# Performance work log

Hardware: AMD Instinct MI355X
Metric: run time of the kernel (lower is better)

## Reference

```python
import jax, jax.numpy as jnp
import numpy as np

CUBE_SIZE = 24
N_NEURONS = CUBE_SIZE ** 3  # 13824
INPUT_DIM = 512
OUTPUT_DIM = 1000
MAX_STEPS = 30
BATCH = 256


def _build_neighbor_indices(size: int) -> np.ndarray:
    """[N, 27] int32; invalid (out-of-cube) neighbors map to pad slot N."""
    n = size ** 3
    c = np.arange(size)
    z, y, x = np.meshgrid(c, c, c, indexing='ij')  # each [size,size,size]
    cols = []
    for dz in (-1, 0, 1):
        for dy in (-1, 0, 1):
            for dx in (-1, 0, 1):
                nz, ny, nx = z + dz, y + dy, x + dx
                valid = ((nz >= 0) & (nz < size) & (ny >= 0) & (ny < size)
                         & (nx >= 0) & (nx < size))
                idx = nz * size * size + ny * size + nx
                cols.append(np.where(valid, idx, n))
    return np.stack(cols, axis=-1).reshape(n, 27).astype(np.int32)


def setup_inputs() -> dict:
    key = jax.random.key(0)
    ks = jax.random.split(key, 4)
    # xavier-ish small init scales (gain 0.5 style)
    w_in = jax.random.normal(ks[0], (N_NEURONS, INPUT_DIM), jnp.float32) * 0.01
    w_local = jax.random.normal(ks[1], (N_NEURONS, 27), jnp.float32) * 0.1
    w_out = jax.random.normal(ks[2], (OUTPUT_DIM, N_NEURONS), jnp.float32) * 0.01
    x = jax.random.normal(ks[3], (BATCH, INPUT_DIM), jnp.float32)
    return {
        'x': x,
        'W_in_w': w_in,
        'W_in_b': jnp.zeros((N_NEURONS,), jnp.float32),
        'W_local': w_local,
        'W_out_w': w_out,
        'W_out_b': jnp.zeros((OUTPUT_DIM,), jnp.float32),
        'neighbor_indices': jnp.asarray(_build_neighbor_indices(CUBE_SIZE)),
    }


def reference(x, W_in_w, W_in_b, W_local, W_out_w, W_out_b, neighbor_indices):
    batch = x.shape[0]
    x_proj = x @ W_in_w.T + W_in_b  # [B, N]
    h0 = jnp.zeros((batch, N_NEURONS), x.dtype)
    pad = jnp.zeros((batch, 1), x.dtype)

    def step(h, _):
        h_padded = jnp.concatenate([h, pad], axis=1)        # [B, N+1]
        nbr = h_padded[:, neighbor_indices]                  # [B, N, 27]
        weighted = jnp.einsum('bnk,nk->bn', nbr, W_local)    # [B, N]
        return jnp.tanh(x_proj + weighted), None

    h, _ = jax.lax.scan(step, h0, None, length=MAX_STEPS)
    return h @ W_out_w.T + W_out_b  # [B, output_dim]
```

## Files before the change

### kernel.cpp

```cpp
#include <hip/hip_runtime.h>

#define NN   13824
#define BB   256
#define KDIM 512
#define ODIM 1000
#define CUBE 24
#define KS   16

typedef short bf8 __attribute__((ext_vector_type(8)));
typedef float f32x4 __attribute__((ext_vector_type(4)));

__device__ __forceinline__ float fast_tanh(float a) {
    float e = __expf(2.0f * a);
    return 1.0f - 2.0f / (e + 1.0f);
}
__device__ __forceinline__ float bf_lo(unsigned u) { return __uint_as_float(u << 16); }
__device__ __forceinline__ float bf_hi(unsigned u) { return __uint_as_float(u & 0xffff0000u); }
__device__ __forceinline__ unsigned short bf_rne(float f) {
    unsigned u = __float_as_uint(f);
    u += 0x7fffu + ((u >> 16) & 1u);
    return (unsigned short)(u >> 16);
}
__device__ __forceinline__ unsigned bf_pack(float lo, float hi) {
    return (unsigned)bf_rne(lo) | ((unsigned)bf_rne(hi) << 16);
}
__device__ __forceinline__ bf8 cvt8(float4 a, float4 b) {
    bf8 r;
    r[0] = (short)bf_rne(a.x); r[1] = (short)bf_rne(a.y);
    r[2] = (short)bf_rne(a.z); r[3] = (short)bf_rne(a.w);
    r[4] = (short)bf_rne(b.x); r[5] = (short)bf_rne(b.y);
    r[6] = (short)bf_rne(b.z); r[7] = (short)bf_rne(b.w);
    return r;
}

__global__ __launch_bounds__(256) void xbf_kernel(
    const float* __restrict__ x, unsigned* __restrict__ xb)
{
    int i = blockIdx.x * 256 + threadIdx.x;
    float2 v = *(const float2*)&x[(size_t)i * 2];
    xb[i] = bf_pack(v.x, v.y);
}

__global__ __launch_bounds__(256) void xproj_mfma(
    const float* __restrict__ w_in, const float* __restrict__ bias,
    const short* __restrict__ xbf, unsigned short* __restrict__ xp)
{
    const int tid = threadIdx.x, w = tid >> 6, lane = tid & 63;
    const int quad = lane >> 4, l16 = lane & 15;
    const int n0 = blockIdx.x * 16;
    const float* __restrict__ arow = &w_in[(size_t)(n0 + l16) * KDIM];

    f32x4 acc[4] = {};
    for (int k0 = 0; k0 < KDIM; k0 += 32) {
        const int ka = k0 + quad * 8;
        float4 a0 = *(const float4*)&arow[ka];
        float4 a1 = *(const float4*)&arow[ka + 4];
        bf8 af = cvt8(a0, a1);
#pragma unroll
        for (int j = 0; j < 4; ++j) {
            const int b = w * 64 + j * 16 + l16;
            bf8 bfr = *(const bf8*)&xbf[(size_t)b * KDIM + ka];
            acc[j] = __builtin_amdgcn_mfma_f32_16x16x32_bf16(af, bfr, acc[j], 0, 0, 0);
        }
    }
#pragma unroll
    for (int j = 0; j < 4; ++j) {
        const int b = w * 64 + j * 16 + l16;
#pragma unroll
        for (int r = 0; r < 4; ++r) {
            const int n = n0 + quad * 4 + r;
            xp[(size_t)n * BB + b] = bf_rne(acc[j][r] + bias[n]);
        }
    }
}

__global__ __launch_bounds__(256) void init_kernel(
    const unsigned* __restrict__ xp, unsigned* __restrict__ h)
{
    int i = (blockIdx.x * 256 + threadIdx.x) * 4;
    uint4 v = *(const uint4*)&xp[i];
    uint4 o;
    o.x = bf_pack(fast_tanh(bf_lo(v.x)), fast_tanh(bf_hi(v.x)));
    o.y = bf_pack(fast_tanh(bf_lo(v.y)), fast_tanh(bf_hi(v.y)));
    o.z = bf_pack(fast_tanh(bf_lo(v.z)), fast_tanh(bf_hi(v.z)));
    o.w = bf_pack(fast_tanh(bf_lo(v.w)), fast_tanh(bf_hi(v.w)));
    *(uint4*)&h[i] = o;
}

__device__ __forceinline__ void load_plane_u(
    const unsigned* __restrict__ h32, int z, int y, int xx, int dof, unsigned* w9)
{
#pragma unroll
    for (int j = 0; j < 9; ++j) {
        const int dz = j / 3 - 1, dy = j % 3 - 1;
        const int zz = z + dz, yy = y + dy;
        const bool valid = (xx >= 0) & (xx < CUBE) & (zz >= 0) & (zz < CUBE) &
                           (yy >= 0) & (yy < CUBE);
        unsigned v = 0u;
        if (valid) v = h32[(size_t)((zz * 24 + yy) * 24 + xx) * 128 + dof];
        w9[j] = v;
    }
}

__global__ __launch_bounds__(256) void step_kernel(
    const unsigned* __restrict__ hprev, const unsigned* __restrict__ xp,
    const float* __restrict__ wl, unsigned* __restrict__ hnext)
{
    const int tid  = threadIdx.x;
    const int wv   = __builtin_amdgcn_readfirstlane(tid >> 6);
    const int lane = tid & 63;

    const int bid   = blockIdx.x;
    const int zhi   = bid & 7;
    const int inner = bid >> 3;
    const int y     = inner % 24;
    const int r     = inner / 24;
    const int zlo   = r % 3;
    const int xcp   = r / 3;
    const int z     = zhi * 3 + zlo;

    const int xc   = xcp * 2 + (wv & 1);
    const int x0   = xc * 6;
    const int dof  = (wv >> 1) * 64 + lane;

    unsigned win[5][9];
    load_plane_u(hprev, z, y, x0 - 1, dof, win[0]);
    load_plane_u(hprev, z, y, x0,     dof, win[1]);
    load_plane_u(hprev, z, y, x0 + 1, dof, win[2]);
    load_plane_u(hprev, z, y, x0 + 2, dof, win[3]);

#pragma unroll
    for (int xi = 0; xi < 6; ++xi) {
        const int x = x0 + xi;
        if (xi <= 3)
            load_plane_u(hprev, z, y, x + 3, dof, win[(xi + 4) % 5]);

        const int n = (z * 24 + y) * 24 + x;
        const float* __restrict__ wn = &wl[(size_t)n * 27];
        const unsigned xpv = xp[(size_t)n * 128 + dof];
        float acc0 = bf_lo(xpv), acc1 = bf_hi(xpv);

        const unsigned* pm = win[xi % 5];
        const unsigned* pc = win[(xi + 1) % 5];
        const unsigned* pp = win[(xi + 2) % 5];
#pragma unroll
        for (int j = 0; j < 9; ++j) {
            const float w0 = wn[3 * j + 0];
            const float w1 = wn[3 * j + 1];
            const float w2 = wn[3 * j + 2];
            acc0 += w0 * bf_lo(pm[j]) + w1 * bf_lo(pc[j]) + w2 * bf_lo(pp[j]);
            acc1 += w0 * bf_hi(pm[j]) + w1 * bf_hi(pc[j]) + w2 * bf_hi(pp[j]);
        }
        hnext[(size_t)n * 128 + dof] = bf_pack(fast_tanh(acc0), fast_tanh(acc1));
    }
}

__global__ __launch_bounds__(256) void transpose_kernel(
    const unsigned* __restrict__ h32, unsigned* __restrict__ hT32)
{
    __shared__ unsigned short T[64][66];
    const int tid = threadIdx.x;
    const int rr = tid >> 2, g = tid & 3;
    const int k0 = blockIdx.x * 64, b0 = blockIdx.y * 64;
#pragma unroll
    for (int i = 0; i < 8; ++i) {
        unsigned d = h32[(size_t)(k0 + rr) * 128 + b0 / 2 + g * 8 + i];
        const int bl = (g * 8 + i) * 2;
        T[bl][rr]     = (unsigned short)(d & 0xffffu);
        T[bl + 1][rr] = (unsigned short)(d >> 16);
    }
    __syncthreads();
#pragma unroll
    for (int i = 0; i < 8; ++i) {
        const int kl = (g * 8 + i) * 2;
        unsigned d = (unsigned)T[rr][kl] | ((unsigned)T[rr][kl + 1] << 16);
        hT32[(size_t)(b0 + rr) * (NN / 2) + k0 / 2 + g * 8 + i] = d;
    }
}

__global__ __launch_bounds__(256) void outgemm_mfma(
    const float* __restrict__ wout, const short* __restrict__ hT,
    float* __restrict__ part)
{
    const int tid = threadIdx.x, w = tid >> 6, lane = tid & 63;
    const int quad = lane >> 4, l16 = lane & 15;
    const int o0 = blockIdx.x * 32 + (w & 1) * 16;
    const int bh = w >> 1;
    const int kb = blockIdx.y * (NN / KS);
    const int o_row = o0 + l16;
    const bool aval = o_row < ODIM;
    const float* __restrict__ arow = &wout[(size_t)o_row * NN];

    f32x4 acc[8] = {};
    for (int ki = 0; ki < NN / KS; ki += 32) {
        const int ka = kb + ki + quad * 8;
        bf8 af = {};
        if (aval) {
            float4 a0 = *(const float4*)&arow[ka];
            float4 a1 = *(const float4*)&arow[ka + 4];
            af = cvt8(a0, a1);
        }
#pragma unroll
        for (int j = 0; j < 8; ++j) {
            const int b = bh * 128 + j * 16 + l16;
            bf8 bfr = *(const bf8*)&hT[(size_t)b * NN + ka];
            acc[j] = __builtin_amdgcn_mfma_f32_16x16x32_bf16(af, bfr, acc[j], 0, 0, 0);
        }
    }
#pragma unroll
    for (int j = 0; j < 8; ++j) {
        const int b = bh * 128 + j * 16 + l16;
#pragma unroll
        for (int r = 0; r < 4; ++r) {
            const int o = o0 + quad * 4 + r;
            part[((size_t)blockIdx.y * 1024 + o) * BB + b] = acc[j][r];
        }
    }
}

__global__ __launch_bounds__(256) void reduce_kernel(
    const float* __restrict__ part, const float* __restrict__ bias,
    float* __restrict__ out)
{
    const int o = blockIdx.x, b = threadIdx.x;
    float s = bias[o];
#pragma unroll
    for (int kc = 0; kc < KS; ++kc)
        s += part[((size_t)kc * 1024 + o) * BB + b];
    out[(size_t)b * ODIM + o] = s;
}

extern "C" void kernel_launch(void* const* d_in, const int* in_sizes, int n_in,
                              void* d_out, int out_size, void* d_ws, size_t ws_size,
                              hipStream_t stream)
{
    const float* x       = (const float*)d_in[0];
    const float* w_in    = (const float*)d_in[1];
    const float* b_in    = (const float*)d_in[2];
    const float* w_local = (const float*)d_in[3];
    const float* w_out   = (const float*)d_in[4];
    const float* b_out   = (const float*)d_in[5];
    float* out = (float*)d_out;

    char* p = (char*)d_ws;
    unsigned short* xp_bf = (unsigned short*)p;          p += (size_t)NN * BB * 2;
    unsigned short* hA    = (unsigned short*)p;          p += (size_t)NN * BB * 2;
    unsigned short* hB    = (unsigned short*)p;          p += (size_t)NN * BB * 2;
    unsigned short* hT    = (unsigned short*)p;          p += (size_t)NN * BB * 2;
    unsigned short* x_bf  = (unsigned short*)p;          p += (size_t)BB * KDIM * 2;
    float*          part  = (float*)p;

    xbf_kernel<<<256, 256, 0, stream>>>(x, (unsigned*)x_bf);
    xproj_mfma<<<864, 256, 0, stream>>>(w_in, b_in, (const short*)x_bf, xp_bf);
    init_kernel<<<1728, 256, 0, stream>>>((const unsigned*)xp_bf, (unsigned*)hA);

    const unsigned* hp = (const unsigned*)hA;
    unsigned* hn = (unsigned*)hB;
    for (int s = 0; s < 29; ++s) {
        step_kernel<<<1152, 256, 0, stream>>>(hp, (const unsigned*)xp_bf, w_local, hn);
        unsigned* t = (unsigned*)hp; hp = hn; hn = t;
    }

    transpose_kernel<<<dim3(216, 4), 256, 0, stream>>>(hp, (unsigned*)hT);
    outgemm_mfma<<<dim3(32, KS), 256, 0, stream>>>(w_out, (const short*)hT, part);
    reduce_kernel<<<ODIM, 256, 0, stream>>>(part, b_out, out);
}
```

Baseline: 598.4 us.

## Fuse init tanh into xproj, prefetch GEMM operands, shrink step blocks

The tanh initialisation kernel is folded into the input projection epilogue, which removes one launch and one pass over memory. Both MFMA GEMMs now software-prefetch the next K-slice into registers. The output GEMM is retiled so each wave covers two 16-row output tiles and reuses its B fragments across them. The step kernel moves to 128-thread blocks with twice as many blocks and unpacks bf16 neighbours to float2 once at load time. Packing now uses the HIP bf16 intrinsic, and the extra prefetch registers may lower occupancy.

```diff
diff --git a/kernel.cpp b/kernel.cpp
--- a/kernel.cpp
+++ b/kernel.cpp
@@ -1,4 +1,5 @@
 #include <hip/hip_runtime.h>
+#include <hip/hip_bf16.h>
 
 #define NN   13824
 #define BB   256
@@ -21,16 +22,18 @@
     u += 0x7fffu + ((u >> 16) & 1u);
     return (unsigned short)(u >> 16);
 }
-__device__ __forceinline__ unsigned bf_pack(float lo, float hi) {
-    return (unsigned)bf_rne(lo) | ((unsigned)bf_rne(hi) << 16);
+__device__ __forceinline__ unsigned pk_bf16(float lo, float hi) {
+    union { __hip_bfloat162 h; unsigned u; } cv;
+    cv.h = __float22bfloat162_rn(make_float2(lo, hi));
+    return cv.u;
 }
 __device__ __forceinline__ bf8 cvt8(float4 a, float4 b) {
-    bf8 r;
-    r[0] = (short)bf_rne(a.x); r[1] = (short)bf_rne(a.y);
-    r[2] = (short)bf_rne(a.z); r[3] = (short)bf_rne(a.w);
-    r[4] = (short)bf_rne(b.x); r[5] = (short)bf_rne(b.y);
-    r[6] = (short)bf_rne(b.z); r[7] = (short)bf_rne(b.w);
-    return r;
+    union { bf8 v; unsigned u[4]; } r;
+    r.u[0] = pk_bf16(a.x, a.y);
+    r.u[1] = pk_bf16(a.z, a.w);
+    r.u[2] = pk_bf16(b.x, b.y);
+    r.u[3] = pk_bf16(b.z, b.w);
+    return r.v;
 }
 
 __global__ __launch_bounds__(256) void xbf_kernel(
@@ -38,12 +41,13 @@
 {
     int i = blockIdx.x * 256 + threadIdx.x;
     float2 v = *(const float2*)&x[(size_t)i * 2];
-    xb[i] = bf_pack(v.x, v.y);
+    xb[i] = pk_bf16(v.x, v.y);
 }
 
 __global__ __launch_bounds__(256) void xproj_mfma(
     const float* __restrict__ w_in, const float* __restrict__ bias,
-    const short* __restrict__ xbf, unsigned short* __restrict__ xp)
+    const short* __restrict__ xbf, unsigned short* __restrict__ xp,
+    unsigned short* __restrict__ h1)
 {
     const int tid = threadIdx.x, w = tid >> 6, lane = tid & 63;
     const int quad = lane >> 4, l16 = lane & 15;
@@ -51,44 +55,50 @@
     const float* __restrict__ arow = &w_in[(size_t)(n0 + l16) * KDIM];
 
     f32x4 acc[4] = {};
-    for (int k0 = 0; k0 < KDIM; k0 += 32) {
-        const int ka = k0 + quad * 8;
-        float4 a0 = *(const float4*)&arow[ka];
-        float4 a1 = *(const float4*)&arow[ka + 4];
+
+    int ka = quad * 8;
+    float4 a0 = *(const float4*)&arow[ka];
+    float4 a1 = *(const float4*)&arow[ka + 4];
+    bf8 bb[4];
+#pragma unroll
+    for (int j = 0; j < 4; ++j)
+        bb[j] = *(const bf8*)&xbf[(size_t)(w * 64 + j * 16 + l16) * KDIM + ka];
+
+    for (int it = 0; it < 16; ++it) {
+        float4 na0{}, na1{}; bf8 nb[4] = {};
+        if (it < 15) {
+            const int nka = ka + 32;
+            na0 = *(const float4*)&arow[nka];
+            na1 = *(const float4*)&arow[nka + 4];
+#pragma unroll
+            for (int j = 0; j < 4; ++j)
+                nb[j] = *(const bf8*)&xbf[(size_t)(w * 64 + j * 16 + l16) * KDIM + nka];
+        }
         bf8 af = cvt8(a0, a1);
 #pragma unroll
-        for (int j = 0; j < 4; ++j) {
-            const int b = w * 64 + j * 16 + l16;
-            bf8 bfr = *(const bf8*)&xbf[(size_t)b * KDIM + ka];
-            acc[j] = __builtin_amdgcn_mfma_f32_16x16x32_bf16(af, bfr, acc[j], 0, 0, 0);
-        }
-    }
+        for (int j = 0; j < 4; ++j)
+            acc[j] = __builtin_amdgcn_mfma_f32_16x16x32_bf16(af, bb[j], acc[j], 0, 0, 0);
+        a0 = na0; a1 = na1;
+#pragma unroll
+        for (int j = 0; j < 4; ++j) bb[j] = nb[j];
+        ka += 32;
+    }
+
 #pragma unroll
     for (int j = 0; j < 4; ++j) {
         const int b = w * 64 + j * 16 + l16;
 #pragma unroll
         for (int r = 0; r < 4; ++r) {
             const int n = n0 + quad * 4 + r;
-            xp[(size_t)n * BB + b] = bf_rne(acc[j][r] + bias[n]);
-        }
-    }
-}
-
-__global__ __launch_bounds__(256) void init_kernel(
-    const unsigned* __restrict__ xp, unsigned* __restrict__ h)
-{
-    int i = (blockIdx.x * 256 + threadIdx.x) * 4;
-    uint4 v = *(const uint4*)&xp[i];
-    uint4 o;
-    o.x = bf_pack(fast_tanh(bf_lo(v.x)), fast_tanh(bf_hi(v.x)));
-    o.y = bf_pack(fast_tanh(bf_lo(v.y)), fast_tanh(bf_hi(v.y)));
-    o.z = bf_pack(fast_tanh(bf_lo(v.z)), fast_tanh(bf_hi(v.z)));
-    o.w = bf_pack(fast_tanh(bf_lo(v.w)), fast_tanh(bf_hi(v.w)));
-    *(uint4*)&h[i] = o;
-}
-
-__device__ __forceinline__ void load_plane_u(
-    const unsigned* __restrict__ h32, int z, int y, int xx, int dof, unsigned* w9)
+            const float v = acc[j][r] + bias[n];
+            xp[(size_t)n * BB + b] = bf_rne(v);
+            h1[(size_t)n * BB + b] = bf_rne(fast_tanh(v));
+        }
+    }
+}
+
+__device__ __forceinline__ void load_plane_f2(
+    const unsigned* __restrict__ h32, int z, int y, int xx, int dof, float2* w9)
 {
 #pragma unroll
     for (int j = 0; j < 9; ++j) {
@@ -98,11 +108,11 @@
                            (yy >= 0) & (yy < CUBE);
         unsigned v = 0u;
         if (valid) v = h32[(size_t)((zz * 24 + yy) * 24 + xx) * 128 + dof];
-        w9[j] = v;
-    }
-}
-
-__global__ __launch_bounds__(256) void step_kernel(
+        w9[j] = make_float2(bf_lo(v), bf_hi(v));
+    }
+}
+
+__global__ __launch_bounds__(128) void step_kernel(
     const unsigned* __restrict__ hprev, const unsigned* __restrict__ xp,
     const float* __restrict__ wl, unsigned* __restrict__ hnext)
 {
@@ -115,43 +125,42 @@
     const int inner = bid >> 3;
     const int y     = inner % 24;
     const int r     = inner / 24;
-    const int zlo   = r % 3;
-    const int xcp   = r / 3;
+    const int xc    = r & 3;
+    const int zlo   = r >> 2;
     const int z     = zhi * 3 + zlo;
 
-    const int xc   = xcp * 2 + (wv & 1);
     const int x0   = xc * 6;
-    const int dof  = (wv >> 1) * 64 + lane;
-
-    unsigned win[5][9];
-    load_plane_u(hprev, z, y, x0 - 1, dof, win[0]);
-    load_plane_u(hprev, z, y, x0,     dof, win[1]);
-    load_plane_u(hprev, z, y, x0 + 1, dof, win[2]);
-    load_plane_u(hprev, z, y, x0 + 2, dof, win[3]);
+    const int dof  = wv * 64 + lane;
+
+    float2 win[5][9];
+    load_plane_f2(hprev, z, y, x0 - 1, dof, win[0]);
+    load_plane_f2(hprev, z, y, x0,     dof, win[1]);
+    load_plane_f2(hprev, z, y, x0 + 1, dof, win[2]);
+    load_plane_f2(hprev, z, y, x0 + 2, dof, win[3]);
 
 #pragma unroll
     for (int xi = 0; xi < 6; ++xi) {
         const int x = x0 + xi;
         if (xi <= 3)
-            load_plane_u(hprev, z, y, x + 3, dof, win[(xi + 4) % 5]);
+            load_plane_f2(hprev, z, y, x + 3, dof, win[(xi + 4) % 5]);
 
         const int n = (z * 24 + y) * 24 + x;
         const float* __restrict__ wn = &wl[(size_t)n * 27];
         const unsigned xpv = xp[(size_t)n * 128 + dof];
-        float acc0 = bf_lo(xpv), acc1 = bf_hi(xpv);
-
-        const unsigned* pm = win[xi % 5];
-        const unsigned* pc = win[(xi + 1) % 5];
-        const unsigned* pp = win[(xi + 2) % 5];
+        float2 acc = make_float2(bf_lo(xpv), bf_hi(xpv));
+
+        const float2* pm = win[xi % 5];
+        const float2* pc = win[(xi + 1) % 5];
+        const float2* pp = win[(xi + 2) % 5];
 #pragma unroll
         for (int j = 0; j < 9; ++j) {
             const float w0 = wn[3 * j + 0];
             const float w1 = wn[3 * j + 1];
             const float w2 = wn[3 * j + 2];
-            acc0 += w0 * bf_lo(pm[j]) + w1 * bf_lo(pc[j]) + w2 * bf_lo(pp[j]);
-            acc1 += w0 * bf_hi(pm[j]) + w1 * bf_hi(pc[j]) + w2 * bf_hi(pp[j]);
-        }
-        hnext[(size_t)n * 128 + dof] = bf_pack(fast_tanh(acc0), fast_tanh(acc1));
+            acc.x += w0 * pm[j].x + w1 * pc[j].x + w2 * pp[j].x;
+            acc.y += w0 * pm[j].y + w1 * pc[j].y + w2 * pp[j].y;
+        }
+        hnext[(size_t)n * 128 + dof] = pk_bf16(fast_tanh(acc.x), fast_tanh(acc.y));
     }
 }
 
@@ -184,38 +193,64 @@
 {
     const int tid = threadIdx.x, w = tid >> 6, lane = tid & 63;
     const int quad = lane >> 4, l16 = lane & 15;
-    const int o0 = blockIdx.x * 32 + (w & 1) * 16;
-    const int bh = w >> 1;
+    const int o0 = blockIdx.x * 32;
     const int kb = blockIdx.y * (NN / KS);
-    const int o_row = o0 + l16;
-    const bool aval = o_row < ODIM;
-    const float* __restrict__ arow = &wout[(size_t)o_row * NN];
-
-    f32x4 acc[8] = {};
-    for (int ki = 0; ki < NN / KS; ki += 32) {
-        const int ka = kb + ki + quad * 8;
-        bf8 af = {};
-        if (aval) {
-            float4 a0 = *(const float4*)&arow[ka];
-            float4 a1 = *(const float4*)&arow[ka + 4];
-            af = cvt8(a0, a1);
-        }
-#pragma unroll
-        for (int j = 0; j < 8; ++j) {
-            const int b = bh * 128 + j * 16 + l16;
-            bf8 bfr = *(const bf8*)&hT[(size_t)b * NN + ka];
-            acc[j] = __builtin_amdgcn_mfma_f32_16x16x32_bf16(af, bfr, acc[j], 0, 0, 0);
-        }
-    }
-#pragma unroll
-    for (int j = 0; j < 8; ++j) {
-        const int b = bh * 128 + j * 16 + l16;
-#pragma unroll
-        for (int r = 0; r < 4; ++r) {
-            const int o = o0 + quad * 4 + r;
-            part[((size_t)blockIdx.y * 1024 + o) * BB + b] = acc[j][r];
-        }
-    }
+    const int b0 = w * 64;
+
+    const int oa = o0 + l16, ob = o0 + 16 + l16;
+    const bool av0 = oa < ODIM, av1 = ob < ODIM;
+    const float* __restrict__ ar0 = &wout[(size_t)oa * NN];
+    const float* __restrict__ ar1 = &wout[(size_t)ob * NN];
+    const float4 z4 = {0.f, 0.f, 0.f, 0.f};
+
+    f32x4 acc[2][4] = {};
+
+    int ka = kb + quad * 8;
+    float4 a00 = av0 ? *(const float4*)&ar0[ka]     : z4;
+    float4 a01 = av0 ? *(const float4*)&ar0[ka + 4] : z4;
+    float4 a10 = av1 ? *(const float4*)&ar1[ka]     : z4;
+    float4 a11 = av1 ? *(const float4*)&ar1[ka + 4] : z4;
+    bf8 bb[4];
+#pragma unroll
+    for (int j = 0; j < 4; ++j)
+        bb[j] = *(const bf8*)&hT[(size_t)(b0 + j * 16 + l16) * NN + ka];
+
+    for (int it = 0; it < 27; ++it) {
+        float4 na00{}, na01{}, na10{}, na11{}; bf8 nb[4] = {};
+        if (it < 26) {
+            const int nka = ka + 32;
+            na00 = av0 ? *(const float4*)&ar0[nka]     : z4;
+            na01 = av0 ? *(const float4*)&ar0[nka + 4] : z4;
+            na10 = av1 ? *(const float4*)&ar1[nka]     : z4;
+            na11 = av1 ? *(const float4*)&ar1[nka + 4] : z4;
+#pragma unroll
+            for (int j = 0; j < 4; ++j)
+                nb[j] = *(const bf8*)&hT[(size_t)(b0 + j * 16 + l16) * NN + nka];
+        }
+        bf8 af0 = cvt8(a00, a01);
+        bf8 af1 = cvt8(a10, a11);
+#pragma unroll
+        for (int j = 0; j < 4; ++j) {
+            acc[0][j] = __builtin_amdgcn_mfma_f32_16x16x32_bf16(af0, bb[j], acc[0][j], 0, 0, 0);
+            acc[1][j] = __builtin_amdgcn_mfma_f32_16x16x32_bf16(af1, bb[j], acc[1][j], 0, 0, 0);
+        }
+        a00 = na00; a01 = na01; a10 = na10; a11 = na11;
+#pragma unroll
+        for (int j = 0; j < 4; ++j) bb[j] = nb[j];
+        ka += 32;
+    }
+
+#pragma unroll
+    for (int i = 0; i < 2; ++i)
+#pragma unroll
+        for (int j = 0; j < 4; ++j) {
+            const int b = b0 + j * 16 + l16;
+#pragma unroll
+            for (int r = 0; r < 4; ++r) {
+                const int o = o0 + i * 16 + quad * 4 + r;
+                part[((size_t)blockIdx.y * 1024 + o) * BB + b] = acc[i][j][r];
+            }
+        }
 }
 
 __global__ __launch_bounds__(256) void reduce_kernel(
@@ -251,13 +286,12 @@
     float*          part  = (float*)p;
 
     xbf_kernel<<<256, 256, 0, stream>>>(x, (unsigned*)x_bf);
-    xproj_mfma<<<864, 256, 0, stream>>>(w_in, b_in, (const short*)x_bf, xp_bf);
-    init_kernel<<<1728, 256, 0, stream>>>((const unsigned*)xp_bf, (unsigned*)hA);
+    xproj_mfma<<<864, 256, 0, stream>>>(w_in, b_in, (const short*)x_bf, xp_bf, hA);
 
     const unsigned* hp = (const unsigned*)hA;
     unsigned* hn = (unsigned*)hB;
     for (int s = 0; s < 29; ++s) {
-        step_kernel<<<1152, 256, 0, stream>>>(hp, (const unsigned*)xp_bf, w_local, hn);
+        step_kernel<<<2304, 128, 0, stream>>>(hp, (const unsigned*)xp_bf, w_local, hn);
         unsigned* t = (unsigned*)hp; hp = hn; hn = t;
     }
 
```

Result: faster. 573.4 us (-4.2%).
